# Kernel tuning notes

Hardware: AMD Instinct MI355X
Metric: run time of the kernel (lower is better)

## Reference

```python
import jax, jax.numpy as jnp
import numpy as np
import math

SEQ, BSZ, D, H, W = 2048, 2, 1024, 16, 8
HD = D // H          # head_dim = 64
P = SEQ // W         # phrase_num = 256 (seq divisible by window -> no pad needed)


def setup_inputs() -> dict:
    key = jax.random.key(0)
    ks = jax.random.split(key, 8)
    s = 1.0 / math.sqrt(D)
    def w(k):
        return jax.random.normal(k, (D, D), jnp.float32) * s
    zb = jnp.zeros((D,), jnp.float32)
    return {
        'query': jax.random.normal(ks[0], (SEQ, BSZ, D), jnp.float32),
        'Wq_base': w(ks[1]), 'bq_base': zb,
        'Wk_base': w(ks[2]), 'bk_base': zb,
        'Wq_gauss': w(ks[3]), 'bq_gauss': zb,
        'Wk_gauss': w(ks[4]), 'bk_gauss': zb,
        'Wv': w(ks[5]), 'bv': zb,
        'Wo': w(ks[6]), 'bo': zb,
    }


def reference(query, Wq_base, bq_base, Wk_base, bk_base,
              Wq_gauss, bq_gauss, Wk_gauss, bk_gauss, Wv, bv, Wo, bo):
    seq, bsz, d = query.shape
    scaling = HD ** -0.5

    def to_heads(x):  # (len, bsz, D) -> (bsz, H, len, HD)
        return x.reshape(x.shape[0], bsz, H, HD).transpose(1, 2, 0, 3)

    # ---- base multi-head attention branch ----
    q_b = to_heads(query @ Wq_base.T + bq_base) * scaling
    k_b = to_heads(query @ Wk_base.T + bk_base)
    v = to_heads(query @ Wv.T + bv)
    base_scores = jnp.einsum('bhid,bhjd->bhij', q_b, k_b)   # (B,H,S,S)
    attn_base = jax.nn.softmax(base_scores, axis=-1)

    # ---- phrase encoding: fixed windows + max pooling ----
    phrase = query.reshape(P, W, bsz, d).max(axis=1)        # (P, bsz, D)

    # ---- gaussian branch: query attends over phrase reps ----
    q_g = to_heads(query @ Wq_gauss.T + bq_gauss) * scaling
    k_g = (phrase @ Wk_gauss.T + bk_gauss).reshape(P, bsz, H, HD).transpose(1, 2, 0, 3)
    wts = jax.nn.softmax(jnp.einsum('bhid,bhpd->bhip', q_g, k_g), axis=-1)  # (B,H,S,P)

    # fixed Gaussians per phrase: mu at window center, sigma = window/4
    pos = jnp.arange(seq, dtype=jnp.float32)                     # key positions
    mu = jnp.arange(P, dtype=jnp.float32) * W + (W - 1) / 2.0    # (P,)
    sigma = W / 4.0
    gauss = jnp.exp(-(pos[None, :] - mu[:, None]) ** 2 / (2.0 * sigma * sigma)) \
            / (math.sqrt(2.0 * math.pi) * sigma)                 # (P, S)
    attn_gauss = jnp.einsum('bhip,pj->bhij', wts, gauss)         # (B,H,S,S)

    # combine the two attention distributions
    attn = 0.5 * (attn_base + attn_gauss)

    out = jnp.einsum('bhij,bhjd->bhid', attn, v)                 # (B,H,S,HD)
    out = out.transpose(2, 0, 1, 3).reshape(seq, bsz, d)         # (S,B,D)
    return out @ Wo.T + bo
```

## Files before the change

### kernel.cpp

```cpp
#include <hip/hip_runtime.h>
#include <hip/hip_bf16.h>

#define SEQ 2048
#define BSZ 2
#define DIM 1024
#define NH 16
#define HD 64
#define WIN 8
#define PN 256

typedef __hip_bfloat16 bf16;
typedef __attribute__((ext_vector_type(8))) short short8;
typedef __attribute__((ext_vector_type(4))) short short4v;
typedef __attribute__((ext_vector_type(2))) unsigned int uint2v;
typedef __attribute__((ext_vector_type(4))) float f32x4;

__device__ __forceinline__ float b2f(bf16 x) { return __bfloat162float(x); }
__device__ __forceinline__ bf16 f2b(float x) { return __float2bfloat16(x); }
__device__ __forceinline__ short fbits(float x) { bf16 h = __float2bfloat16(x); return *(short*)&h; }

__device__ __forceinline__ unsigned pk2bf(float lo, float hi) {
    return __builtin_amdgcn_perm(__float_as_uint(hi) + 0x8000u,
                                 __float_as_uint(lo) + 0x8000u, 0x07060302u);
}

__device__ __forceinline__ void gl_lds16(const bf16* g, bf16* l) {
    __builtin_amdgcn_global_load_lds((const __attribute__((address_space(1))) void*)g,
                                     (__attribute__((address_space(3))) void*)l, 16, 0, 0);
}

__device__ __forceinline__ bf16* swzp(bf16* base, int row, int byteoff) {
    return (bf16*)((char*)base + (row << 7) + (byteoff ^ ((row & 7) << 4)));
}

__global__ void convert_kernel(const float* __restrict__ q,
                               const float* __restrict__ w0, const float* __restrict__ w1,
                               const float* __restrict__ w2, const float* __restrict__ w3,
                               const float* __restrict__ w4, const float* __restrict__ w5,
                               const float* __restrict__ b0, const float* __restrict__ b1,
                               const float* __restrict__ b2, const float* __restrict__ b3,
                               const float* __restrict__ b4, const float* __restrict__ b5,
                               bf16* __restrict__ qbf, bf16* __restrict__ wbf,
                               float* __restrict__ bp) {
    int i = blockIdx.x * 256 + threadIdx.x;
    const int QV = (SEQ * BSZ * DIM) / 8;
    const int WV = (DIM * DIM) / 8;
    const int TV = QV + 6 * WV;
    if (i >= TV) {
        int j = i - TV;
        if (j >= 768) return;
        int mat = j >> 7, k = (j & 127) * 8;
        const float* s = (mat == 0) ? b0 : (mat == 1) ? b1 : (mat == 2) ? b2
                       : (mat == 3) ? b3 : (mat == 4) ? b4 : b5;
        *(f32x4*)(bp + mat * DIM + k)     = *(const f32x4*)(s + k);
        *(f32x4*)(bp + mat * DIM + k + 4) = *(const f32x4*)(s + k + 4);
        return;
    }
    const float* src;
    bf16* dst;
    size_t off;
    if (i < QV) { src = q; dst = qbf; off = (size_t)i * 8; }
    else {
        int j = i - QV;
        int mat = j / WV, k = j - mat * WV;
        src = (mat == 0) ? w0 : (mat == 1) ? w1 : (mat == 2) ? w2
            : (mat == 3) ? w3 : (mat == 4) ? w4 : w5;
        dst = wbf + (size_t)mat * DIM * DIM;
        off = (size_t)k * 8;
    }
    f32x4 av4 = *(const f32x4*)(src + off);
    f32x4 bv4 = *(const f32x4*)(src + off + 4);
    short8 o;
#pragma unroll
    for (int e = 0; e < 4; ++e) { o[e] = fbits(av4[e]); o[e + 4] = fbits(bv4[e]); }
    *(short8*)(dst + off) = o;
}

__global__ void phrase_max_kernel(const float* __restrict__ q, bf16* __restrict__ phrase) {
    int idx = blockIdx.x * 256 + threadIdx.x;
    int d  = idx % DIM;
    int pb = idx / DIM;
    int b  = pb % BSZ;
    int p  = pb / BSZ;
    float m = -1e30f;
#pragma unroll
    for (int w = 0; w < WIN; ++w)
        m = fmaxf(m, q[((size_t)(p * WIN + w) * BSZ + b) * DIM + d]);
    phrase[idx] = f2b(m);
}

__global__ void gauss_v_kernel(const bf16* __restrict__ vT, bf16* __restrict__ gvT) {
    int row = blockIdx.x;
    int p   = threadIdx.x;
    float mu = p * (float)WIN + (WIN - 1) * 0.5f;
    float acc = 0.f;
    int j0 = p * WIN - 12;
    const bf16* src = vT + (size_t)row * SEQ;
#pragma unroll
    for (int jj = 0; jj < 32; ++jj) {
        int j = j0 + jj;
        if (j < 0 || j >= SEQ) continue;
        float dd = (float)j - mu;
        acc += __expf(-dd * dd * 0.125f) * 0.199471140200716f * b2f(src[j]);
    }
    gvT[(size_t)row * PN + p] = f2b(acc);
}

__device__ __forceinline__ void gemm_body(const bf16* __restrict__ A,
                                          const bf16* __restrict__ W,
                                          const float* __restrict__ bias,
                                          void* __restrict__ Cout,
                                          int m0, int n0, float scale,
                                          int mode, int LEN) {
    __shared__ bf16 As[128 * 32];
    __shared__ bf16 Ws[128 * 32];
    int t = threadIdx.x;
    int wave = t >> 6, lane = t & 63;
    int wm = (wave >> 1) * 64, wn = (wave & 1) * 64;
    int l15 = lane & 15, quad = lane >> 4;

    f32x4 acc[4][4] = {};

    for (int k0 = 0; k0 < DIM; k0 += 32) {
        {
            int c0 = t, c1 = t + 256;
            gl_lds16(A + (size_t)(m0 + (c0 >> 2)) * DIM + k0 + (c0 & 3) * 8, &As[c0 * 8]);
            gl_lds16(A + (size_t)(m0 + (c1 >> 2)) * DIM + k0 + (c1 & 3) * 8, &As[c1 * 8]);
            gl_lds16(W + (size_t)(n0 + (c0 >> 2)) * DIM + k0 + (c0 & 3) * 8, &Ws[c0 * 8]);
            gl_lds16(W + (size_t)(n0 + (c1 >> 2)) * DIM + k0 + (c1 & 3) * 8, &Ws[c1 * 8]);
        }
        __syncthreads();
        short8 af[4], bfr[4];
#pragma unroll
        for (int tm = 0; tm < 4; ++tm)
            af[tm] = *(short8*)&As[(wm + tm * 16 + l15) * 32 + quad * 8];
#pragma unroll
        for (int tn = 0; tn < 4; ++tn)
            bfr[tn] = *(short8*)&Ws[(wn + tn * 16 + l15) * 32 + quad * 8];
#pragma unroll
        for (int tm = 0; tm < 4; ++tm)
#pragma unroll
            for (int tn = 0; tn < 4; ++tn)
                acc[tm][tn] = __builtin_amdgcn_mfma_f32_16x16x32_bf16(af[tm], bfr[tn], acc[tm][tn], 0, 0, 0);
        __syncthreads();
    }

#pragma unroll
    for (int tm = 0; tm < 4; ++tm) {
        int mrow = m0 + wm + tm * 16 + quad * 4;
#pragma unroll
        for (int tn = 0; tn < 4; ++tn) {
            int n = n0 + wn + tn * 16 + l15;
            float bsv = bias[n];
#pragma unroll
            for (int r = 0; r < 4; ++r) {
                int m = mrow + r;
                float val = (acc[tm][tn][r] + bsv) * scale;
                int s = m / BSZ, b = m % BSZ;
                int h = n >> 6, hd = n & 63;
                if (mode == 0)
                    ((bf16*)Cout)[((size_t)(b * NH + h) * LEN + s) * HD + hd] = f2b(val);
                else
                    ((bf16*)Cout)[((size_t)(b * NH + h) * HD + hd) * LEN + s] = f2b(val);
            }
        }
    }
}

#define QSCALE (0.125f * 1.44269504088896f)

__global__ __launch_bounds__(256) void gemm_proj(const bf16* __restrict__ qbf,
                                                 const bf16* __restrict__ phrasebf,
                                                 const bf16* __restrict__ wbf,
                                                 const float* __restrict__ bias_pack,
                                                 bf16* __restrict__ q_b, bf16* __restrict__ k_b,
                                                 bf16* __restrict__ vT, bf16* __restrict__ q_g,
                                                 bf16* __restrict__ k_g) {
    int z = blockIdx.z;
    const bf16* A = qbf;
    bf16* C;
    int mode = 0, LEN = SEQ;
    float scale = 1.0f;
    switch (z) {
        case 0: C = q_b; scale = QSCALE; break;
        case 1: C = k_b; break;
        case 2: C = vT; mode = 2; break;
        case 3: C = q_g; scale = QSCALE; break;
        default:
            if (blockIdx.x >= 4) return;
            A = phrasebf; C = k_g; LEN = PN; break;
    }
    gemm_body(A, wbf + (size_t)z * DIM * DIM, bias_pack + z * DIM, C,
              blockIdx.x * 128, blockIdx.y * 128, scale, mode, LEN);
}

__global__ __launch_bounds__(256) void gemm_final(const bf16* __restrict__ A,
                                                  const bf16* __restrict__ wbf,
                                                  const float* __restrict__ bias_pack,
                                                  float* __restrict__ out) {
    __shared__ bf16 As[64 * 32];
    __shared__ bf16 Ws[128 * 32];
    const bf16* W = wbf + (size_t)5 * DIM * DIM;
    const float* bias = bias_pack + 5 * DIM;
    int t = threadIdx.x;
    int m0 = blockIdx.x * 64, n0 = blockIdx.y * 128;
    int wave = t >> 6, lane = t & 63;
    int wm = (wave >> 1) * 32, wn = (wave & 1) * 64;
    int l15 = lane & 15, quad = lane >> 4;

    f32x4 acc[2][4] = {};

    for (int k0 = 0; k0 < DIM; k0 += 32) {
        {
            int c0 = t, c1 = t + 256;
            gl_lds16(A + (size_t)(m0 + (c0 >> 2)) * DIM + k0 + (c0 & 3) * 8, &As[c0 * 8]);
            gl_lds16(W + (size_t)(n0 + (c0 >> 2)) * DIM + k0 + (c0 & 3) * 8, &Ws[c0 * 8]);
            gl_lds16(W + (size_t)(n0 + (c1 >> 2)) * DIM + k0 + (c1 & 3) * 8, &Ws[c1 * 8]);
        }
        __syncthreads();
        short8 af[2], bfr[4];
#pragma unroll
        for (int tm = 0; tm < 2; ++tm)
            af[tm] = *(short8*)&As[(wm + tm * 16 + l15) * 32 + quad * 8];
#pragma unroll
        for (int tn = 0; tn < 4; ++tn)
            bfr[tn] = *(short8*)&Ws[(wn + tn * 16 + l15) * 32 + quad * 8];
#pragma unroll
        for (int tm = 0; tm < 2; ++tm)
#pragma unroll
            for (int tn = 0; tn < 4; ++tn)
                acc[tm][tn] = __builtin_amdgcn_mfma_f32_16x16x32_bf16(af[tm], bfr[tn], acc[tm][tn], 0, 0, 0);
        __syncthreads();
    }

#pragma unroll
    for (int tm = 0; tm < 2; ++tm) {
        int mrow = m0 + wm + tm * 16 + quad * 4;
#pragma unroll
        for (int tn = 0; tn < 4; ++tn) {
            int n = n0 + wn + tn * 16 + l15;
            float bsv = bias[n];
#pragma unroll
            for (int r = 0; r < 4; ++r)
                out[(size_t)(mrow + r) * DIM + n] = acc[tm][tn][r] + bsv;
        }
    }
}

__global__ __launch_bounds__(128) void attn_kernel(const bf16* __restrict__ qb,
                                                   const bf16* __restrict__ kb,
                                                   const bf16* __restrict__ vT,
                                                   const bf16* __restrict__ qg,
                                                   const bf16* __restrict__ kg,
                                                   const bf16* __restrict__ gvT,
                                                   bf16* __restrict__ out) {
    __shared__ bf16 QPs[64 * 64];
    __shared__ bf16 Ks[64 * 64];
    __shared__ bf16 Vt[64 * 64];

    int t = threadIdx.x;
    int wave = t >> 6, lane = t & 63;
    int l15 = lane & 15, quad = lane >> 4;
    int flat = blockIdx.y * gridDim.x + blockIdx.x;
    int wid = (flat & 7) * 128 + (flat >> 3);
    int q0 = (wid & 31) * 64;
    int bh = wid >> 5;
    int b = bh / NH, h = bh % NH;

    const short8 ones = (short8)0x3F80;

    float result[2][4][4] = {};

    for (int phase = 0; phase < 2; ++phase) {
        const bf16* qptr = phase ? qb : qg;
        const bf16* kptr = phase ? kb : kg;
        const bf16* vtp  = phase ? vT : gvT;
        int kvlen = phase ? SEQ : PN;
        int nchunk = kvlen / 64;

        __syncthreads();
        {
            int r = t >> 1, cb = (t & 1) * 64;
            const bf16* qsrc = qptr + ((size_t)bh * SEQ + q0 + r) * HD + (t & 1) * 32;
            *(short8*)swzp(QPs, r, cb)      = *(const short8*)(qsrc);
            *(short8*)swzp(QPs, r, cb + 16) = *(const short8*)(qsrc + 8);
            *(short8*)swzp(QPs, r, cb + 32) = *(const short8*)(qsrc + 16);
            *(short8*)swzp(QPs, r, cb + 48) = *(const short8*)(qsrc + 24);
        }
        __syncthreads();
        short8 bq[2][2];
#pragma unroll
        for (int qt = 0; qt < 2; ++qt) {
            int r = wave * 32 + qt * 16 + l15;
            bq[qt][0] = *(short8*)swzp(QPs, r, quad * 16);
            bq[qt][1] = *(short8*)swzp(QPs, r, 64 + quad * 16);
        }

        int sr = t >> 1, sb = (t & 1) * 64;
        const bf16* kbase = kptr + ((size_t)bh * kvlen + sr) * HD + (t & 1) * 32;
        const bf16* vbase = vtp + (size_t)(bh * HD + sr) * kvlen + (t & 1) * 32;

        const bf16* kn = kbase;
        const bf16* vn = vbase;
        short8 kr[4], vr[4];
#pragma unroll
        for (int j = 0; j < 4; ++j) {
            kr[j] = *(const short8*)(kn + j * 8);
            vr[j] = *(const short8*)(vn + j * 8);
        }

        f32x4 o_acc[2][4] = {};
        f32x4 l_acc[2] = {};
        for (int ch = 0; ch < nchunk; ++ch) {
            __syncthreads();
#pragma unroll
            for (int j = 0; j < 4; ++j) {
                *(short8*)swzp(Ks, sr, sb + j * 16) = kr[j];
                *(short8*)swzp(Vt, sr, sb + j * 16) = vr[j];
            }
            if (ch + 1 < nchunk) {
                kn += 64 * HD;
                vn += 64;
#pragma unroll
                for (int j = 0; j < 4; ++j) {
                    kr[j] = *(const short8*)(kn + j * 8);
                    vr[j] = *(const short8*)(vn + j * 8);
                }
            }
            __syncthreads();

            f32x4 s_acc[2][4] = {};
#pragma unroll
            for (int kk = 0; kk < 2; ++kk) {
#pragma unroll
                for (int tn = 0; tn < 4; ++tn) {
                    short8 ak = *(short8*)swzp(Ks, tn * 16 + l15, kk * 64 + quad * 16);
                    s_acc[0][tn] = __builtin_amdgcn_mfma_f32_16x16x32_bf16(ak, bq[0][kk], s_acc[0][tn], 0, 0, 0);
                    s_acc[1][tn] = __builtin_amdgcn_mfma_f32_16x16x32_bf16(ak, bq[1][kk], s_acc[1][tn], 0, 0, 0);
                }
            }
#pragma unroll
            for (int qt = 0; qt < 2; ++qt)
#pragma unroll
                for (int tn = 0; tn < 4; ++tn) {
                    float e0 = __builtin_amdgcn_exp2f(s_acc[qt][tn][0]);
                    float e1 = __builtin_amdgcn_exp2f(s_acc[qt][tn][1]);
                    float e2 = __builtin_amdgcn_exp2f(s_acc[qt][tn][2]);
                    float e3 = __builtin_amdgcn_exp2f(s_acc[qt][tn][3]);
                    uint2v pw;
                    pw[0] = pk2bf(e0, e1);
                    pw[1] = pk2bf(e2, e3);
                    *(uint2v*)swzp(QPs, wave * 32 + qt * 16 + l15, tn * 32 + quad * 8) = pw;
                }
#pragma unroll
            for (int kk = 0; kk < 2; ++kk) {
                short8 pa0 = *(short8*)swzp(QPs, wave * 32 + l15,      kk * 64 + quad * 16);
                short8 pa1 = *(short8*)swzp(QPs, wave * 32 + 16 + l15, kk * 64 + quad * 16);
                l_acc[0] = __builtin_amdgcn_mfma_f32_16x16x32_bf16(pa0, ones, l_acc[0], 0, 0, 0);
                l_acc[1] = __builtin_amdgcn_mfma_f32_16x16x32_bf16(pa1, ones, l_acc[1], 0, 0, 0);
#pragma unroll
                for (int tn = 0; tn < 4; ++tn) {
                    short8 vb = *(short8*)swzp(Vt, tn * 16 + l15, kk * 64 + quad * 16);
                    o_acc[0][tn] = __builtin_amdgcn_mfma_f32_16x16x32_bf16(pa0, vb, o_acc[0][tn], 0, 0, 0);
                    o_acc[1][tn] = __builtin_amdgcn_mfma_f32_16x16x32_bf16(pa1, vb, o_acc[1][tn], 0, 0, 0);
                }
            }
        }
#pragma unroll
        for (int qt = 0; qt < 2; ++qt)
#pragma unroll
            for (int r = 0; r < 4; ++r) {
                float inv = 0.5f / fmaxf(l_acc[qt][r], 1e-30f);
#pragma unroll
                for (int tn = 0; tn < 4; ++tn)
                    result[qt][tn][r] += o_acc[qt][tn][r] * inv;
            }
    }

#pragma unroll
    for (int qt = 0; qt < 2; ++qt)
#pragma unroll
        for (int r = 0; r < 4; ++r) {
            int srow = q0 + wave * 32 + qt * 16 + quad * 4 + r;
            int mm = srow * BSZ + b;
#pragma unroll
            for (int tn = 0; tn < 4; ++tn) {
                int dcol = h * HD + tn * 16 + l15;
                out[(size_t)mm * DIM + dcol] = f2b(result[qt][tn][r]);
            }
        }
}

extern "C" void kernel_launch(void* const* d_in, const int* in_sizes, int n_in,
                              void* d_out, int out_size, void* d_ws, size_t ws_size,
                              hipStream_t stream) {
    (void)in_sizes; (void)n_in; (void)out_size; (void)ws_size;
    const float* query = (const float*)d_in[0];
    const float* Wq_b  = (const float*)d_in[1];
    const float* bq_b  = (const float*)d_in[2];
    const float* Wk_b  = (const float*)d_in[3];
    const float* bk_b  = (const float*)d_in[4];
    const float* Wq_g  = (const float*)d_in[5];
    const float* bq_g  = (const float*)d_in[6];
    const float* Wk_g  = (const float*)d_in[7];
    const float* bk_g  = (const float*)d_in[8];
    const float* Wv    = (const float*)d_in[9];
    const float* bv    = (const float*)d_in[10];
    const float* Wo    = (const float*)d_in[11];
    const float* bo    = (const float*)d_in[12];
    float* out = (float*)d_out;

    const size_t NQ = (size_t)BSZ * NH * SEQ * HD;
    const size_t NP = (size_t)BSZ * NH * PN * HD;
    bf16* qbf      = (bf16*)d_ws;
    bf16* wbf      = qbf + NQ;
    bf16* phrasebf = wbf + (size_t)6 * DIM * DIM;
    bf16* q_b      = phrasebf + (size_t)PN * BSZ * DIM;
    bf16* k_b      = q_b + NQ;
    bf16* vT       = k_b + NQ;
    bf16* q_g      = vT + NQ;
    bf16* k_g      = q_g + NQ;
    bf16* gvT      = k_g + NP;
    bf16* attn_bf  = gvT + NP;
    float* bias_pack = (float*)(attn_bf + NQ);

    const int QV = (SEQ * BSZ * DIM) / 8, WV6 = 6 * (DIM * DIM) / 8;
    convert_kernel<<<(QV + WV6) / 256 + 3, 256, 0, stream>>>(
        query, Wq_b, Wk_b, Wv, Wq_g, Wk_g, Wo,
        bq_b, bk_b, bv, bq_g, bk_g, bo, qbf, wbf, bias_pack);
    phrase_max_kernel<<<(PN * BSZ * DIM) / 256, 256, 0, stream>>>(query, phrasebf);

    dim3 gp((SEQ * BSZ) / 128, DIM / 128, 5);
    gemm_proj<<<gp, 256, 0, stream>>>(qbf, phrasebf, wbf, bias_pack,
                                      q_b, k_b, vT, q_g, k_g);

    gauss_v_kernel<<<BSZ * NH * HD, PN, 0, stream>>>(vT, gvT);

    dim3 g3(SEQ / 64, BSZ * NH);
    attn_kernel<<<g3, 128, 0, stream>>>(q_b, k_b, vT, q_g, k_g, gvT, attn_bf);

    dim3 gf((SEQ * BSZ) / 64, DIM / 128);
    gemm_final<<<gf, 256, 0, stream>>>(attn_bf, wbf, bias_pack, out);
}
```

Measured before the change: 268.7 us.

## Load Q, K and V fragments directly from global memory into MFMA registers

The attention kernel no longer stages Q, K and V tiles through shared memory. Each wave loads its MFMA operand fragments straight from global memory, which removes the block-wide barriers and LDS round trips per chunk, and only the P tile stays in LDS. The cost is that each wave now fetches the K and V tiles itself, doubling global/L2 traffic for those across the two waves. The register prefetch of the next chunk is also gone, so load latency is exposed unless other waves hide it.

```diff
diff --git a/kernel.cpp b/kernel.cpp
--- a/kernel.cpp
+++ b/kernel.cpp
@@ -254,9 +254,7 @@
                                                    const bf16* __restrict__ kg,
                                                    const bf16* __restrict__ gvT,
                                                    bf16* __restrict__ out) {
-    __shared__ bf16 QPs[64 * 64];
-    __shared__ bf16 Ks[64 * 64];
-    __shared__ bf16 Vt[64 * 64];
+    __shared__ bf16 Ps[64 * 64];
 
     int t = threadIdx.x;
     int wave = t >> 6, lane = t & 63;
@@ -278,67 +276,39 @@
         int kvlen = phase ? SEQ : PN;
         int nchunk = kvlen / 64;
 
-        __syncthreads();
-        {
-            int r = t >> 1, cb = (t & 1) * 64;
-            const bf16* qsrc = qptr + ((size_t)bh * SEQ + q0 + r) * HD + (t & 1) * 32;
-            *(short8*)swzp(QPs, r, cb)      = *(const short8*)(qsrc);
-            *(short8*)swzp(QPs, r, cb + 16) = *(const short8*)(qsrc + 8);
-            *(short8*)swzp(QPs, r, cb + 32) = *(const short8*)(qsrc + 16);
-            *(short8*)swzp(QPs, r, cb + 48) = *(const short8*)(qsrc + 24);
-        }
-        __syncthreads();
         short8 bq[2][2];
 #pragma unroll
         for (int qt = 0; qt < 2; ++qt) {
-            int r = wave * 32 + qt * 16 + l15;
-            bq[qt][0] = *(short8*)swzp(QPs, r, quad * 16);
-            bq[qt][1] = *(short8*)swzp(QPs, r, 64 + quad * 16);
-        }
-
-        int sr = t >> 1, sb = (t & 1) * 64;
-        const bf16* kbase = kptr + ((size_t)bh * kvlen + sr) * HD + (t & 1) * 32;
-        const bf16* vbase = vtp + (size_t)(bh * HD + sr) * kvlen + (t & 1) * 32;
-
-        const bf16* kn = kbase;
-        const bf16* vn = vbase;
-        short8 kr[4], vr[4];
-#pragma unroll
-        for (int j = 0; j < 4; ++j) {
-            kr[j] = *(const short8*)(kn + j * 8);
-            vr[j] = *(const short8*)(vn + j * 8);
-        }
+            const bf16* qr = qptr + ((size_t)bh * SEQ + q0 + wave * 32 + qt * 16 + l15) * HD + quad * 8;
+            bq[qt][0] = *(const short8*)(qr);
+            bq[qt][1] = *(const short8*)(qr + 32);
+        }
+
+        const bf16* kf = kptr + ((size_t)bh * kvlen + l15) * HD + quad * 8;
+        const bf16* vf = vtp + ((size_t)(bh * HD) + l15) * kvlen + quad * 8;
 
         f32x4 o_acc[2][4] = {};
         f32x4 l_acc[2] = {};
         for (int ch = 0; ch < nchunk; ++ch) {
-            __syncthreads();
-#pragma unroll
-            for (int j = 0; j < 4; ++j) {
-                *(short8*)swzp(Ks, sr, sb + j * 16) = kr[j];
-                *(short8*)swzp(Vt, sr, sb + j * 16) = vr[j];
-            }
-            if (ch + 1 < nchunk) {
-                kn += 64 * HD;
-                vn += 64;
-#pragma unroll
-                for (int j = 0; j < 4; ++j) {
-                    kr[j] = *(const short8*)(kn + j * 8);
-                    vr[j] = *(const short8*)(vn + j * 8);
+            short8 ak[2][4], vb[2][4];
+#pragma unroll
+            for (int kk = 0; kk < 2; ++kk)
+#pragma unroll
+                for (int tn = 0; tn < 4; ++tn) {
+                    ak[kk][tn] = *(const short8*)(kf + (size_t)(tn * 16) * HD + kk * 32);
+                    vb[kk][tn] = *(const short8*)(vf + (size_t)(tn * 16) * kvlen + kk * 32);
                 }
-            }
-            __syncthreads();
+            kf += 64 * HD;
+            vf += 64;
 
             f32x4 s_acc[2][4] = {};
 #pragma unroll
-            for (int kk = 0; kk < 2; ++kk) {
+            for (int kk = 0; kk < 2; ++kk)
 #pragma unroll
                 for (int tn = 0; tn < 4; ++tn) {
-                    short8 ak = *(short8*)swzp(Ks, tn * 16 + l15, kk * 64 + quad * 16);
-                    s_acc[0][tn] = __builtin_amdgcn_mfma_f32_16x16x32_bf16(ak, bq[0][kk], s_acc[0][tn], 0, 0, 0);
-                    s_acc[1][tn] = __builtin_amdgcn_mfma_f32_16x16x32_bf16(ak, bq[1][kk], s_acc[1][tn], 0, 0, 0);
+                    s_acc[0][tn] = __builtin_amdgcn_mfma_f32_16x16x32_bf16(ak[kk][tn], bq[0][kk], s_acc[0][tn], 0, 0, 0);
+                    s_acc[1][tn] = __builtin_amdgcn_mfma_f32_16x16x32_bf16(ak[kk][tn], bq[1][kk], s_acc[1][tn], 0, 0, 0);
                 }
-            }
 #pragma unroll
             for (int qt = 0; qt < 2; ++qt)
 #pragma unroll
@@ -350,19 +320,18 @@
                     uint2v pw;
                     pw[0] = pk2bf(e0, e1);
                     pw[1] = pk2bf(e2, e3);
-                    *(uint2v*)swzp(QPs, wave * 32 + qt * 16 + l15, tn * 32 + quad * 8) = pw;
+                    *(uint2v*)swzp(Ps, wave * 32 + qt * 16 + l15, tn * 32 + quad * 8) = pw;
                 }
 #pragma unroll
             for (int kk = 0; kk < 2; ++kk) {
-                short8 pa0 = *(short8*)swzp(QPs, wave * 32 + l15,      kk * 64 + quad * 16);
-                short8 pa1 = *(short8*)swzp(QPs, wave * 32 + 16 + l15, kk * 64 + quad * 16);
+                short8 pa0 = *(short8*)swzp(Ps, wave * 32 + l15,      kk * 64 + quad * 16);
+                short8 pa1 = *(short8*)swzp(Ps, wave * 32 + 16 + l15, kk * 64 + quad * 16);
                 l_acc[0] = __builtin_amdgcn_mfma_f32_16x16x32_bf16(pa0, ones, l_acc[0], 0, 0, 0);
                 l_acc[1] = __builtin_amdgcn_mfma_f32_16x16x32_bf16(pa1, ones, l_acc[1], 0, 0, 0);
 #pragma unroll
                 for (int tn = 0; tn < 4; ++tn) {
-                    short8 vb = *(short8*)swzp(Vt, tn * 16 + l15, kk * 64 + quad * 16);
-                    o_acc[0][tn] = __builtin_amdgcn_mfma_f32_16x16x32_bf16(pa0, vb, o_acc[0][tn], 0, 0, 0);
-                    o_acc[1][tn] = __builtin_amdgcn_mfma_f32_16x16x32_bf16(pa1, vb, o_acc[1][tn], 0, 0, 0);
+                    o_acc[0][tn] = __builtin_amdgcn_mfma_f32_16x16x32_bf16(pa0, vb[kk][tn], o_acc[0][tn], 0, 0, 0);
+                    o_acc[1][tn] = __builtin_amdgcn_mfma_f32_16x16x32_bf16(pa1, vb[kk][tn], o_acc[1][tn], 0, 0, 0);
                 }
             }
         }
```

After: 373.7 us. 39.1% more time.
